# Kernel tuning notes

Hardware: AMD Instinct MI355X
Metric: run time of the kernel (lower is better)

Reference implementation:

```python
import jax, jax.numpy as jnp
import numpy as np

B, L, D, H = 8, 512, 1024, 16
HD = D // H  # head dim = 64
SCALE = 1.0  # scale=False in __init__


def _rel_sinusoid(seq_len, dim):
    # RelativeSinusoidalPositionalEmbedding lookup for relative positions
    # arange(-L/2, L/2) (even L), sinusoid of the raw relative position.
    half = dim // 2
    inv = jnp.exp(jnp.arange(half, dtype=jnp.float32) * (-(np.log(10000.0) / (half - 1))))
    r = jnp.arange(-(seq_len // 2), seq_len // 2, dtype=jnp.float32)  # (L,)
    ang = r[:, None] * inv[None, :]  # (L, half)
    return jnp.concatenate([jnp.sin(ang), jnp.cos(ang)], axis=1)  # (L, dim)


def setup_inputs() -> dict:
    key = jax.random.key(0)
    ks = jax.random.split(key, 8)
    s = 0.02
    x = jax.random.normal(ks[0], (B, L, D), jnp.float32)
    mask = jax.random.randint(ks[1], (B, L), 0, 2).astype(jnp.int64)
    mask = mask.at[:, 0].set(1)  # ensure at least one valid key per row
    qmask = jax.random.randint(ks[2], (B, L), 0, 2).astype(jnp.int64)
    w_qkv = jax.random.normal(ks[3], (D, 3 * D), jnp.float32) * s
    w_qkpos = jax.random.normal(ks[4], (HD, 2 * D), jnp.float32) * s
    w_fc = jax.random.normal(ks[5], (D, D), jnp.float32) * s
    b_fc = jnp.zeros((D,), jnp.float32)
    shift = jnp.abs(jax.random.normal(ks[6], (1,), jnp.float32)) + 0.001
    bias = -jnp.abs(jax.random.normal(ks[7], (1,), jnp.float32))
    return dict(x=x, mask=mask, qmask=qmask, w_qkv=w_qkv, w_qkpos=w_qkpos,
                w_fc=w_fc, b_fc=b_fc, shift=shift, bias=bias)


def reference(x, mask, qmask, w_qkv, w_qkpos, w_fc, b_fc, shift, bias):
    # trans_type='self', use_Gaussian=True, dropout in eval mode (identity)
    b, l, d = x.shape
    qkv = x @ w_qkv  # (B, L, 3D)
    q, k, v = jnp.split(qkv, 3, axis=-1)
    q = q.reshape(b, l, H, HD).transpose(0, 2, 1, 3)  # (B,H,L,hd)
    k = k.reshape(b, l, H, HD).transpose(0, 2, 1, 3)
    v = v.reshape(b, l, H, HD).transpose(0, 2, 1, 3)

    pe = _rel_sinusoid(l, HD)               # (L, hd)
    y = pe @ w_qkpos                        # (L, 2D)
    q_p, k_p = jnp.split(y, 2, axis=-1)     # (L, D) each
    q_p = q_p.reshape(l, H, HD).transpose(1, 0, 2)  # (H, L, hd)
    k_p = k_p.reshape(l, H, HD).transpose(1, 0, 2)  # (H, L, hd)

    attn = jnp.einsum('bhid,bhjd->bhij', q, k) + jnp.einsum('hid,hjd->hij', q_p, k_p)[None]

    # speaker-identity masking: zero out cross-speaker scores (trans_type='self')
    qsame = qmask[:, :, None] == qmask[:, None, :]  # (B, L, L)
    attn = jnp.where(qsame[:, None], attn, 0.0)
    attn = attn / SCALE

    # key padding mask -> -inf
    attn = jnp.where(mask[:, None, None, :] == 0, -jnp.inf, attn)

    # Gaussian distance bias: -(shift * (i-j)^2 + bias)
    idx = jnp.arange(l, dtype=jnp.float32)
    sqd = (idx[:, None] - idx[None, :]) ** 2  # (L, L)
    attn = attn + (-(shift[0] * sqd + bias[0]))[None, None]

    attn = jax.nn.softmax(attn, axis=-1)
    out = jnp.einsum('bhij,bhjd->bhid', attn, v)  # (B,H,L,hd)
    out = out.transpose(0, 2, 1, 3).reshape(b, l, d)
    return out @ w_fc + b_fc
```

## Files before the change

kernel.cpp:

```cpp
#include <hip/hip_runtime.h>
#include <hip/hip_bf16.h>

#define BB 8
#define LL 512
#define DD 1024
#define HH 16
#define HD 64
#define LOG2E 1.4426950408889634f

typedef __attribute__((ext_vector_type(8))) unsigned short u16x8;
typedef __attribute__((ext_vector_type(4))) unsigned short u16x4;
typedef __attribute__((ext_vector_type(8))) __bf16 bf16x8;
typedef __attribute__((ext_vector_type(4))) float f32x4;
typedef __attribute__((ext_vector_type(16))) float f32x16;

#define DEV __device__ __forceinline__

DEV unsigned short f2bf(float f) {
    return __builtin_bit_cast(unsigned short, (__bf16)f);
}
DEV f32x4 mfma16(u16x8 a, u16x8 b, f32x4 c) {
    return __builtin_amdgcn_mfma_f32_16x16x32_bf16(
        __builtin_bit_cast(bf16x8, a), __builtin_bit_cast(bf16x8, b), c, 0, 0, 0);
}
DEV f32x16 mfma32(u16x8 a, u16x8 b, f32x16 c) {
    return __builtin_amdgcn_mfma_f32_32x32x16_bf16(
        __builtin_bit_cast(bf16x8, a), __builtin_bit_cast(bf16x8, b), c, 0, 0, 0);
}
DEV u16x8 v8pair(const unsigned short* a, const unsigned short* b) {
    u16x4 x = *(const u16x4*)a;
    u16x4 y = *(const u16x4*)b;
    u16x8 r;
    r[0] = x[0]; r[1] = x[1]; r[2] = x[2]; r[3] = x[3];
    r[4] = y[0]; r[5] = y[1]; r[6] = y[2]; r[7] = y[3];
    return r;
}
typedef __attribute__((address_space(1))) void gv_t;
typedef __attribute__((address_space(3))) void lv_t;
DEV void gload16(const void* g, void* l) {
    __builtin_amdgcn_global_load_lds((gv_t*)g, (lv_t*)l, 16, 0, 0);
}

__global__ __launch_bounds__(256) void cvt_x(const float* __restrict__ in,
                                             unsigned short* __restrict__ out) {
    int i = blockIdx.x * 256 + threadIdx.x;
    f32x4 v = *(const f32x4*)(in + i * 4);
    u16x4 o;
    o[0] = f2bf(v[0]); o[1] = f2bf(v[1]); o[2] = f2bf(v[2]); o[3] = f2bf(v[3]);
    *(u16x4*)(out + i * 4) = o;
}

__global__ __launch_bounds__(256) void transpose_cvt(
    const float* __restrict__ in, unsigned short* __restrict__ out,
    int R, int C) {
    __shared__ unsigned short tile[32][33];
    int c0 = blockIdx.x * 32, r0 = blockIdx.y * 32;
    int tx = threadIdx.x & 31, ty = threadIdx.x >> 5;
#pragma unroll
    for (int i = 0; i < 32; i += 8)
        tile[ty + i][tx] = f2bf(in[(r0 + ty + i) * C + c0 + tx]);
    __syncthreads();
#pragma unroll
    for (int i = 0; i < 32; i += 8)
        out[(c0 + ty + i) * R + r0 + tx] = tile[tx][ty + i];
}

__global__ __launch_bounds__(256) void posg(
    const float* __restrict__ w, unsigned short* __restrict__ qp,
    unsigned short* __restrict__ kp) {
    __shared__ float peS[64][64];
    __shared__ float wS[64][32];
    int c0 = blockIdx.x * 32, i0 = blockIdx.y * 64;
    int t = threadIdx.x;
#pragma unroll
    for (int j = 0; j < 16; ++j) {
        int o = t + j * 256;
        int ri = o >> 6, d = o & 63, dd = d & 31;
        float inv = expf((float)dd * -0.2971077539347156f);
        float ang = (float)(i0 + ri - 256) * inv;
        peS[ri][d] = (d < 32) ? sinf(ang) : cosf(ang);
    }
#pragma unroll
    for (int j = 0; j < 8; ++j) {
        int o = t + j * 256;
        wS[o >> 5][o & 31] = w[(o >> 5) * 2048 + c0 + (o & 31)];
    }
    __syncthreads();
#pragma unroll
    for (int j = 0; j < 8; ++j) {
        int o = t + j * 256;
        int row = o >> 5, col = o & 31;
        float acc = 0.0f;
#pragma unroll
        for (int k = 0; k < 64; ++k) acc += peS[row][k] * wS[k][col];
        int c = c0 + col, i = i0 + row;
        if (c < 1024) qp[i * 1024 + c] = f2bf(acc * LOG2E);
        else          kp[i * 1024 + (c - 1024)] = f2bf(acc);
    }
}

template <int MODE>
__global__ __launch_bounds__(256) void gemm_bt(
    const unsigned short* __restrict__ A, const unsigned short* __restrict__ Bt,
    int M, int N, int K, int NBX, unsigned short* __restrict__ o0,
    unsigned short* __restrict__ o1, unsigned short* __restrict__ o2,
    float* __restrict__ fout, const float* __restrict__ bias) {
    __shared__ __align__(16) unsigned short As[128 * 32];
    __shared__ __align__(16) unsigned short Bs[128 * 32];
    int g = blockIdx.x;
    int swz = (g & 7) * (gridDim.x >> 3) + (g >> 3);
    int bx = swz % NBX, by = swz / NBX;
    int m0 = by * 128, n0 = bx * 128;
    int t = threadIdx.x;
    int w = t >> 6, l = t & 63, lg = l >> 4, lc = l & 15;
    int wr = w >> 1, wc = w & 1;

    f32x4 acc[4][4] = {};

    int sr = w * 16 + (l >> 2);
    int sk = (l & 3) * 8;
    const unsigned short* Ab = A + (m0 + sr) * K + sk;
    const unsigned short* Bb = Bt + (n0 + sr) * K + sk;
    unsigned short* dA0 = As + w * 512;
    unsigned short* dA1 = As + 2048 + w * 512;
    unsigned short* dB0 = Bs + w * 512;
    unsigned short* dB1 = Bs + 2048 + w * 512;

    for (int k0 = 0; k0 < K; k0 += 32) {
        __syncthreads();
        gload16(Ab + k0, dA0);
        gload16(Ab + 64 * K + k0, dA1);
        gload16(Bb + k0, dB0);
        gload16(Bb + 64 * K + k0, dB1);
        __syncthreads();
        u16x8 af[4], bf[4];
#pragma unroll
        for (int mm = 0; mm < 4; ++mm)
            af[mm] = *(const u16x8*)&As[(wr * 64 + mm * 16 + lc) * 32 + lg * 8];
#pragma unroll
        for (int nn = 0; nn < 4; ++nn)
            bf[nn] = *(const u16x8*)&Bs[(wc * 64 + nn * 16 + lc) * 32 + lg * 8];
#pragma unroll
        for (int mm = 0; mm < 4; ++mm)
#pragma unroll
            for (int nn = 0; nn < 4; ++nn)
                acc[mm][nn] = mfma16(af[mm], bf[nn], acc[mm][nn]);
    }

#pragma unroll
    for (int mm = 0; mm < 4; ++mm)
#pragma unroll
        for (int nn = 0; nn < 4; ++nn)
#pragma unroll
            for (int r = 0; r < 4; ++r) {
                int row = m0 + wr * 64 + mm * 16 + lg * 4 + r;
                int col = n0 + wc * 64 + nn * 16 + lc;
                float v = acc[mm][nn][r];
                if (MODE == 0) {
                    int bb = row >> 9, i = row & 511;
                    int which = col >> 10, dd = col & 1023;
                    int hh = dd >> 6, hd = dd & 63;
                    if (which == 0)
                        o0[((bb * HH + hh) * LL + i) * HD + hd] = f2bf(v * LOG2E);
                    else if (which == 1)
                        o1[((bb * HH + hh) * LL + i) * HD + hd] = f2bf(v);
                    else
                        o2[((bb * HH + hh) * HD + hd) * LL + i] = f2bf(v);
                } else {
                    fout[row * N + col] = v + bias[col];
                }
            }
}

__global__ __launch_bounds__(256) void attn_k(
    const unsigned short* __restrict__ Q, const unsigned short* __restrict__ Kt,
    const unsigned short* __restrict__ Vt, const unsigned short* __restrict__ QP,
    const unsigned short* __restrict__ KP, const int* __restrict__ mask,
    const int* __restrict__ qmask, const float* __restrict__ shp,
    unsigned short* __restrict__ out) {
    int g = blockIdx.x;
    int bid = ((g & 7) << 6) + (g >> 3);
    int b = bid >> 6, h = (bid >> 2) & 15, chunk = bid & 3;
    int t = threadIdx.x, w = t >> 6, l = t & 63;
    int lq = l & 31, hi = l >> 5;
    int q = chunk * 128 + w * 32 + lq;
    int bh = b * HH + h;

    u16x8 qf[4], pf[4];
    const unsigned short* Qb = Q + (bh * LL + q) * HD + hi * 8;
    const unsigned short* QPb = QP + q * DD + h * HD + hi * 8;
#pragma unroll
    for (int ks = 0; ks < 4; ++ks) {
        qf[ks] = *(const u16x8*)(Qb + ks * 16);
        pf[ks] = *(const u16x8*)(QPb + ks * 16);
    }

    unsigned long long km[8], qm[8];
#pragma unroll
    for (int t8 = 0; t8 < 8; ++t8) {
        km[t8] = __ballot(mask[b * LL + t8 * 64 + l] != 0);
        qm[t8] = __ballot(qmask[b * LL + t8 * 64 + l] != 0);
    }
    int qi = (qmask[b * LL + q] != 0) ? 1 : 0;

    const float M0 = -1.0e30f, NEGF = -3.0e38f, THR = 8.0f;
    float negs = -(*shp) * LOG2E;
    float m = M0, ls = 0.0f;
    f32x16 o0 = {}, o1 = {};
    float fq = (float)(q - 4 * hi);

    for (int tt = 0; tt < 16; ++tt) {
        const unsigned short* kb = Kt + (bh * LL + tt * 32 + lq) * HD + hi * 8;
        const unsigned short* kpb = KP + (tt * 32 + lq) * DD + h * HD + hi * 8;
        f32x16 s = {};
#pragma unroll
        for (int ks = 0; ks < 4; ++ks)
            s = mfma32(*(const u16x8*)(kb + ks * 16), qf[ks], s);
#pragma unroll
        for (int ks = 0; ks < 4; ++ks)
            s = mfma32(*(const u16x8*)(kpb + ks * 16), pf[ks], s);

        unsigned kwn = ((unsigned)(km[tt >> 1] >> ((tt & 1) * 32))) >> (hi * 4);
        unsigned qwn = ((unsigned)(qm[tt >> 1] >> ((tt & 1) * 32))) >> (hi * 4);
        float bt = fq - 32.0f * (float)tt;
        float p[16];
#pragma unroll
        for (int r = 0; r < 16; ++r) {
            const int off = (r & 3) + 8 * (r >> 2);
            float v = s[r];
            v = (((qwn >> off) & 1u) == (unsigned)qi) ? v : 0.0f;
            float dr = bt - (float)off;
            v = __builtin_fmaf(negs * dr, dr, v);
            v = ((kwn >> off) & 1u) ? v : NEGF;
            p[r] = v;
        }
        float a0 = fmaxf(fmaxf(p[0], p[1]), fmaxf(p[2], p[3]));
        float a1 = fmaxf(fmaxf(p[4], p[5]), fmaxf(p[6], p[7]));
        float a2 = fmaxf(fmaxf(p[8], p[9]), fmaxf(p[10], p[11]));
        float a3 = fmaxf(fmaxf(p[12], p[13]), fmaxf(p[14], p[15]));
        float pmax = fmaxf(fmaxf(a0, a1), fmaxf(a2, a3));
        pmax = fmaxf(pmax, __shfl_xor(pmax, 32));
        if (!__all(pmax <= m + THR)) {
            float mn = fmaxf(m, pmax);
            float sc = __builtin_amdgcn_exp2f(m - mn);
#pragma unroll
            for (int r = 0; r < 16; ++r) { o0[r] *= sc; o1[r] *= sc; }
            ls *= sc;
            m = mn;
        }
#pragma unroll
        for (int r = 0; r < 16; ++r) p[r] = __builtin_amdgcn_exp2f(p[r] - m);
        ls += (((p[0] + p[1]) + (p[2] + p[3])) + ((p[4] + p[5]) + (p[6] + p[7]))) +
              (((p[8] + p[9]) + (p[10] + p[11])) +
               ((p[12] + p[13]) + (p[14] + p[15])));
        u16x8 pf0, pf1;
#pragma unroll
        for (int j = 0; j < 8; ++j) { pf0[j] = f2bf(p[j]); pf1[j] = f2bf(p[8 + j]); }
        const unsigned short* vb0 = Vt + (bh * HD + lq) * LL + tt * 32 + 4 * hi;
        const unsigned short* vb1 = vb0 + 32 * LL;
        o0 = mfma32(v8pair(vb0, vb0 + 8), pf0, o0);
        o0 = mfma32(v8pair(vb0 + 16, vb0 + 24), pf1, o0);
        o1 = mfma32(v8pair(vb1, vb1 + 8), pf0, o1);
        o1 = mfma32(v8pair(vb1 + 16, vb1 + 24), pf1, o1);
    }

    float rs = ls + __shfl_xor(ls, 32);
    float rinv = __builtin_amdgcn_rcpf(rs);
    unsigned short* ob = out + ((long)(b * LL + q)) * DD + h * HD + hi * 4;
#pragma unroll
    for (int rg = 0; rg < 4; ++rg) {
        u16x4 pk0, pk1;
#pragma unroll
        for (int rr = 0; rr < 4; ++rr) {
            pk0[rr] = f2bf(o0[rg * 4 + rr] * rinv);
            pk1[rr] = f2bf(o1[rg * 4 + rr] * rinv);
        }
        *(u16x4*)(ob + rg * 8) = pk0;
        *(u16x4*)(ob + 32 + rg * 8) = pk1;
    }
}

extern "C" void kernel_launch(void* const* d_in, const int* in_sizes, int n_in,
                              void* d_out, int out_size, void* d_ws,
                              size_t ws_size, hipStream_t stream) {
    const float* x     = (const float*)d_in[0];
    const int*   mask  = (const int*)d_in[1];
    const int*   qmask = (const int*)d_in[2];
    const float* w_qkv = (const float*)d_in[3];
    const float* w_qkp = (const float*)d_in[4];
    const float* w_fc  = (const float*)d_in[5];
    const float* b_fc  = (const float*)d_in[6];
    const float* shift = (const float*)d_in[7];

    char* ws = (char*)d_ws;
    unsigned short* xb   = (unsigned short*)(ws);
    unsigned short* qb   = (unsigned short*)(ws + 8388608);
    unsigned short* kb   = (unsigned short*)(ws + 16777216);
    unsigned short* vtb  = (unsigned short*)(ws + 25165824);
    unsigned short* qp   = (unsigned short*)(ws + 33554432);
    unsigned short* kp   = (unsigned short*)(ws + 34603008);
    unsigned short* wqt  = (unsigned short*)(ws + 35651584);
    unsigned short* wft  = (unsigned short*)(ws + 41943040);
    unsigned short* aout = (unsigned short*)(ws + 44040192);

    cvt_x<<<4096, 256, 0, stream>>>(x, xb);
    transpose_cvt<<<dim3(96, 32), 256, 0, stream>>>(w_qkv, wqt, 1024, 3072);
    transpose_cvt<<<dim3(32, 32), 256, 0, stream>>>(w_fc, wft, 1024, 1024);
    posg<<<dim3(64, 8), 256, 0, stream>>>(w_qkp, qp, kp);
    gemm_bt<0><<<768, 256, 0, stream>>>(xb, wqt, 4096, 3072, 1024, 24, qb, kb,
                                        vtb, nullptr, nullptr);
    attn_k<<<512, 256, 0, stream>>>(qb, kb, vtb, qp, kp, mask, qmask, shift,
                                    aout);
    gemm_bt<1><<<256, 256, 0, stream>>>(aout, wft, 4096, 1024, 1024, 8, nullptr,
                                        nullptr, nullptr, (float*)d_out, b_fc);
}
```

Measured before the change: 164.9 us.

## Split attention keys across waves and merge partial softmax via shared memory

The attention kernel now splits each block's key range in half across wave pairs (split-K flash attention), doubling the grid to 1024 blocks with 64 queries each. Partial max, sum and output from the second half are merged through shared memory by the first-half waves before writing. It also splits the QK and positional MFMA accumulations into two independent chains for more ILP. The aim is more parallelism and shorter serial loops per wave, at the cost of a sync, LDS traffic and duplicated Q loads.

Measured after the change: 168.0 us. About the same (+1.9%).

```diff
diff --git a/kernel.cpp b/kernel.cpp
--- a/kernel.cpp
+++ b/kernel.cpp
@@ -172,18 +172,23 @@
             }
 }
 
-__global__ __launch_bounds__(256) void attn_k(
+__global__ __launch_bounds__(256, 4) void attn_k(
     const unsigned short* __restrict__ Q, const unsigned short* __restrict__ Kt,
     const unsigned short* __restrict__ Vt, const unsigned short* __restrict__ QP,
     const unsigned short* __restrict__ KP, const int* __restrict__ mask,
     const int* __restrict__ qmask, const float* __restrict__ shp,
     unsigned short* __restrict__ out) {
+    __shared__ float mbuf[2][64];
+    __shared__ float lsbuf[2][64];
+    __shared__ float obuf[2][64][33];
+
     int g = blockIdx.x;
-    int bid = ((g & 7) << 6) + (g >> 3);
-    int b = bid >> 6, h = (bid >> 2) & 15, chunk = bid & 3;
+    int bid = ((g & 7) << 7) + (g >> 3);
+    int b = bid >> 7, h = (bid >> 3) & 15, qc = bid & 7;
     int t = threadIdx.x, w = t >> 6, l = t & 63;
+    int qg = w & 1, kh = w >> 1;
     int lq = l & 31, hi = l >> 5;
-    int q = chunk * 128 + w * 32 + lq;
+    int q = qc * 64 + qg * 32 + lq;
     int bh = b * HH + h;
 
     u16x8 qf[4], pf[4];
@@ -195,11 +200,12 @@
         pf[ks] = *(const u16x8*)(QPb + ks * 16);
     }
 
-    unsigned long long km[8], qm[8];
-#pragma unroll
-    for (int t8 = 0; t8 < 8; ++t8) {
-        km[t8] = __ballot(mask[b * LL + t8 * 64 + l] != 0);
-        qm[t8] = __ballot(qmask[b * LL + t8 * 64 + l] != 0);
+    unsigned long long km[4], qm[4];
+#pragma unroll
+    for (int t8 = 0; t8 < 4; ++t8) {
+        int base = b * LL + (kh * 4 + t8) * 64 + l;
+        km[t8] = __ballot(mask[base] != 0);
+        qm[t8] = __ballot(qmask[base] != 0);
     }
     int qi = (qmask[b * LL + q] != 0) ? 1 : 0;
 
@@ -209,25 +215,25 @@
     f32x16 o0 = {}, o1 = {};
     float fq = (float)(q - 4 * hi);
 
-    for (int tt = 0; tt < 16; ++tt) {
-        const unsigned short* kb = Kt + (bh * LL + tt * 32 + lq) * HD + hi * 8;
-        const unsigned short* kpb = KP + (tt * 32 + lq) * DD + h * HD + hi * 8;
-        f32x16 s = {};
-#pragma unroll
-        for (int ks = 0; ks < 4; ++ks)
-            s = mfma32(*(const u16x8*)(kb + ks * 16), qf[ks], s);
-#pragma unroll
-        for (int ks = 0; ks < 4; ++ks)
-            s = mfma32(*(const u16x8*)(kpb + ks * 16), pf[ks], s);
+    for (int tt = 0; tt < 8; ++tt) {
+        int ttg = kh * 8 + tt;
+        const unsigned short* kb = Kt + (bh * LL + ttg * 32 + lq) * HD + hi * 8;
+        const unsigned short* kpb = KP + (ttg * 32 + lq) * DD + h * HD + hi * 8;
+        f32x16 sk = {}, sp = {};
+#pragma unroll
+        for (int ks = 0; ks < 4; ++ks) {
+            sk = mfma32(*(const u16x8*)(kb + ks * 16), qf[ks], sk);
+            sp = mfma32(*(const u16x8*)(kpb + ks * 16), pf[ks], sp);
+        }
 
         unsigned kwn = ((unsigned)(km[tt >> 1] >> ((tt & 1) * 32))) >> (hi * 4);
         unsigned qwn = ((unsigned)(qm[tt >> 1] >> ((tt & 1) * 32))) >> (hi * 4);
-        float bt = fq - 32.0f * (float)tt;
+        float bt = fq - 32.0f * (float)ttg;
         float p[16];
 #pragma unroll
         for (int r = 0; r < 16; ++r) {
             const int off = (r & 3) + 8 * (r >> 2);
-            float v = s[r];
+            float v = sk[r] + sp[r];
             v = (((qwn >> off) & 1u) == (unsigned)qi) ? v : 0.0f;
             float dr = bt - (float)off;
             v = __builtin_fmaf(negs * dr, dr, v);
@@ -256,7 +262,7 @@
         u16x8 pf0, pf1;
 #pragma unroll
         for (int j = 0; j < 8; ++j) { pf0[j] = f2bf(p[j]); pf1[j] = f2bf(p[8 + j]); }
-        const unsigned short* vb0 = Vt + (bh * HD + lq) * LL + tt * 32 + 4 * hi;
+        const unsigned short* vb0 = Vt + (bh * HD + lq) * LL + ttg * 32 + 4 * hi;
         const unsigned short* vb1 = vb0 + 32 * LL;
         o0 = mfma32(v8pair(vb0, vb0 + 8), pf0, o0);
         o0 = mfma32(v8pair(vb0 + 16, vb0 + 24), pf1, o0);
@@ -264,19 +270,39 @@
         o1 = mfma32(v8pair(vb1 + 16, vb1 + 24), pf1, o1);
     }
 
-    float rs = ls + __shfl_xor(ls, 32);
-    float rinv = __builtin_amdgcn_rcpf(rs);
-    unsigned short* ob = out + ((long)(b * LL + q)) * DD + h * HD + hi * 4;
-#pragma unroll
-    for (int rg = 0; rg < 4; ++rg) {
-        u16x4 pk0, pk1;
-#pragma unroll
-        for (int rr = 0; rr < 4; ++rr) {
-            pk0[rr] = f2bf(o0[rg * 4 + rr] * rinv);
-            pk1[rr] = f2bf(o1[rg * 4 + rr] * rinv);
-        }
-        *(u16x4*)(ob + rg * 8) = pk0;
-        *(u16x4*)(ob + 32 + rg * 8) = pk1;
+    if (kh == 1) {
+        mbuf[qg][l] = m;
+        lsbuf[qg][l] = ls;
+#pragma unroll
+        for (int r = 0; r < 16; ++r) {
+            obuf[qg][l][r] = o0[r];
+            obuf[qg][l][16 + r] = o1[r];
+        }
+    }
+    __syncthreads();
+    if (kh == 0) {
+        float m1 = mbuf[qg][l], ls1 = lsbuf[qg][l];
+        float mm = fmaxf(m, m1);
+        float sc0 = __builtin_amdgcn_exp2f(m - mm);
+        float sc1 = __builtin_amdgcn_exp2f(m1 - mm);
+        float lsm = ls * sc0 + ls1 * sc1;
+        float rs = lsm + __shfl_xor(lsm, 32);
+        float rinv = __builtin_amdgcn_rcpf(rs);
+        unsigned short* ob = out + ((long)(b * LL + q)) * DD + h * HD + hi * 4;
+#pragma unroll
+        for (int rg = 0; rg < 4; ++rg) {
+            u16x4 pk0, pk1;
+#pragma unroll
+            for (int rr = 0; rr < 4; ++rr) {
+                int i = rg * 4 + rr;
+                float v0 = __builtin_fmaf(o0[i], sc0, obuf[qg][l][i] * sc1);
+                float v1 = __builtin_fmaf(o1[i], sc0, obuf[qg][l][16 + i] * sc1);
+                pk0[rr] = f2bf(v0 * rinv);
+                pk1[rr] = f2bf(v1 * rinv);
+            }
+            *(u16x4*)(ob + rg * 8) = pk0;
+            *(u16x4*)(ob + 32 + rg * 8) = pk1;
+        }
     }
 }
 
@@ -309,8 +335,8 @@
     posg<<<dim3(64, 8), 256, 0, stream>>>(w_qkp, qp, kp);
     gemm_bt<0><<<768, 256, 0, stream>>>(xb, wqt, 4096, 3072, 1024, 24, qb, kb,
                                         vtb, nullptr, nullptr);
-    attn_k<<<512, 256, 0, stream>>>(qb, kb, vtb, qp, kp, mask, qmask, shift,
-                                    aout);
+    attn_k<<<1024, 256, 0, stream>>>(qb, kb, vtb, qp, kp, mask, qmask, shift,
+                                     aout);
     gemm_bt<1><<<256, 256, 0, stream>>>(aout, wft, 4096, 1024, 1024, 8, nullptr,
                                         nullptr, nullptr, (float*)d_out, b_fc);
 }
```
